# Kernel optimization log

Measured on AMD Instinct MI355X. Metric: run time of the kernel, lower is better.

## Reference

```python
import jax, jax.numpy as jnp
import numpy as np

B, S, D, H = 2, 2048, 2048, 16
HD = D // H
ALIBI_BIAS_MAX = 8
NEG_INF = -1e9  # used only via float('-inf') literal below


def build_attn_mask(n_heads, seq_len, alibi_bias_max=8, dtype=jnp.float32):
    # causal mask: -inf strictly above diagonal
    causal = jnp.triu(jnp.full((seq_len, seq_len), -jnp.inf, dtype=dtype), k=1)
    # full alibi bias: -|i-j| scaled per head by 1/2**(m_h)
    rel = jnp.arange(1 - seq_len, 1, dtype=dtype)  # [S]
    bias = rel[None, :] - rel[:, None]             # [S,S]
    bias = -jnp.abs(bias)
    m = jnp.arange(1, n_heads + 1, dtype=dtype) * (alibi_bias_max / n_heads)
    slopes = 1.0 / (2.0 ** m)                      # [H]
    a_bias = bias[None, :, :] * slopes[:, None, None]  # [H,S,S]
    return causal[None, :, :] + a_bias


def setup_inputs() -> dict:
    key = jax.random.key(0)
    ks = jax.random.split(key, 6)
    x = jax.random.normal(ks[0], (B, S, D), dtype=jnp.float32)
    key_padding_mask = jnp.ones((B, S), dtype=bool)  # True = keep (module inverts before torch)
    attn_mask = build_attn_mask(H, S, ALIBI_BIAS_MAX)
    scale = 1.0 / np.sqrt(D)
    in_proj_w = jax.random.normal(ks[1], (3 * D, D), dtype=jnp.float32) * scale
    in_proj_b = jax.random.normal(ks[2], (3 * D,), dtype=jnp.float32) * 0.01
    out_w = jax.random.normal(ks[3], (D, D), dtype=jnp.float32) * scale
    out_b = jax.random.normal(ks[4], (D,), dtype=jnp.float32) * 0.01
    return {"x": x, "key_padding_mask": key_padding_mask, "attn_mask": attn_mask,
            "in_proj_w": in_proj_w, "in_proj_b": in_proj_b,
            "out_w": out_w, "out_b": out_b}


def reference(x, key_padding_mask, attn_mask, in_proj_w, in_proj_b, out_w, out_b):
    # fused QKV projection (torch MultiheadAttention in_proj)
    qkv = jnp.einsum('bsd,ed->bse', x, in_proj_w) + in_proj_b  # [B,S,3D]
    q, k, v = jnp.split(qkv, 3, axis=-1)
    # [B,H,S,hd]
    q = q.reshape(B, S, H, HD).transpose(0, 2, 1, 3)
    k = k.reshape(B, S, H, HD).transpose(0, 2, 1, 3)
    v = v.reshape(B, S, H, HD).transpose(0, 2, 1, 3)
    scores = jnp.einsum('bhqd,bhkd->bhqk', q, k) / jnp.sqrt(jnp.float32(HD))
    scores = scores + attn_mask[None]  # causal + alibi, [1,H,S,S]
    # key_padding_mask True = keep; masked keys -> -inf
    scores = jnp.where(key_padding_mask[:, None, None, :], scores, -jnp.inf)
    attn = jax.nn.softmax(scores, axis=-1)  # [B,H,S,S]
    ctx = jnp.einsum('bhqk,bhkd->bhqd', attn, v)
    ctx = ctx.transpose(0, 2, 1, 3).reshape(B, S, D)
    out = jnp.einsum('bsd,ed->bse', ctx, out_w) + out_b
    # need_weights=True, average_attn_weights default True -> mean over heads
    avg_attn = attn.mean(axis=1)  # [B,S,S]
    return out, avg_attn
```

## Files before the change

kernel.cpp:

```cpp
#include <hip/hip_runtime.h>
#include <math.h>

#define BB 2
#define SS 2048
#define DD 2048
#define HH 16
#define HDIM 128
#define QKVP 6144
#define NEG_INIT  -1.0e30f
#define NEG_CLAMP -3.0e4f

typedef __attribute__((ext_vector_type(8))) short s8v;
typedef __attribute__((ext_vector_type(4))) float f4v;

typedef const unsigned __attribute__((address_space(1)))* gas_ptr;
typedef unsigned __attribute__((address_space(3)))* las_ptr;

__device__ __forceinline__ void gld16(const short* g, short* l) {
  __builtin_amdgcn_global_load_lds((gas_ptr)g, (las_ptr)l, 16, 0, 0);
}

__device__ __forceinline__ short f2bf(float f) {
  unsigned u = __float_as_uint(f);
  unsigned r = (u + 0x7FFFu + ((u >> 16) & 1u)) >> 16;
  return (short)(unsigned short)r;
}

__global__ void conv_bf16(const float* __restrict__ src, short* __restrict__ dst,
                          int n8) {
  int t = blockIdx.x * blockDim.x + threadIdx.x;
  if (t >= n8) return;
  const float* s = src + (size_t)t * 8;
  s8v o;
#pragma unroll
  for (int i = 0; i < 8; i++) o[i] = f2bf(s[i]);
  ((s8v*)dst)[t] = o;
}

template <typename TOUT>
__global__ __launch_bounds__(256) void gemm_bt_bias(
    const short* __restrict__ A, const short* __restrict__ Bm,
    const float* __restrict__ bias, TOUT* __restrict__ C,
    int M, int N, int K)
{
  __shared__ short As[128 * 64];
  __shared__ short Bs[128 * 64];
  const int tid = threadIdx.x;
  const int lane = tid & 63, wid = tid >> 6;
  const int wm = wid >> 1, wn = wid & 1;
  const int ln = lane & 15, quad = lane >> 4;
  const int m0 = blockIdx.y * 128, n0 = blockIdx.x * 128;

  f4v acc[4][4];
#pragma unroll
  for (int i = 0; i < 4; i++)
#pragma unroll
    for (int j = 0; j < 4; j++) acc[i][j] = {0.f, 0.f, 0.f, 0.f};

  const int srow = (lane >> 3);
  const int scol = (lane & 7) * 8;

  for (int kt = 0; kt < K; kt += 64) {
    const short* a_g = A  + (size_t)(m0 + wid * 32 + srow) * K + kt + scol;
    const short* b_g = Bm + (size_t)(n0 + wid * 32 + srow) * K + kt + scol;
    __syncthreads();
#pragma unroll
    for (int i = 0; i < 4; i++) {
      gld16(a_g + (size_t)i * 8 * K, &As[(wid * 32 + i * 8) * 64]);
      gld16(b_g + (size_t)i * 8 * K, &Bs[(wid * 32 + i * 8) * 64]);
    }
    __syncthreads();
#pragma unroll
    for (int kc = 0; kc < 2; kc++) {
      s8v af[4], bfr[4];
#pragma unroll
      for (int i = 0; i < 4; i++)
        af[i] = *(const s8v*)&As[(wm * 64 + i * 16 + ln) * 64 + kc * 32 + quad * 8];
#pragma unroll
      for (int j = 0; j < 4; j++)
        bfr[j] = *(const s8v*)&Bs[(wn * 64 + j * 16 + ln) * 64 + kc * 32 + quad * 8];
#pragma unroll
      for (int i = 0; i < 4; i++)
#pragma unroll
        for (int j = 0; j < 4; j++)
          acc[i][j] = __builtin_amdgcn_mfma_f32_16x16x32_bf16(af[i], bfr[j], acc[i][j], 0, 0, 0);
    }
  }
#pragma unroll
  for (int j = 0; j < 4; j++) {
    int col = n0 + wn * 64 + j * 16 + ln;
    float bv = bias[col];
#pragma unroll
    for (int i = 0; i < 4; i++) {
      int rbase = m0 + wm * 64 + i * 16 + quad * 4;
#pragma unroll
      for (int r = 0; r < 4; r++) {
        float val = acc[i][j][r] + bv;
        if constexpr (sizeof(TOUT) == 4)
          C[(size_t)(rbase + r) * N + col] = val;
        else
          C[(size_t)(rbase + r) * N + col] = f2bf(val);
      }
    }
  }
}

__global__ __launch_bounds__(256) void transpose_v(const short* __restrict__ qkv,
                                                   short* __restrict__ vT) {
  __shared__ short tile[64 * 72];
  const int bh = blockIdx.z;
  const int b = bh >> 4;
  const int hsel = bh & 15;
  const int s0 = blockIdx.x * 64;
  const int hd0 = blockIdx.y * 64;
  const int t = threadIdx.x;
  const int r = t >> 3, c8 = t & 7;
#pragma unroll
  for (int half = 0; half < 2; half++) {
    int rr = r + half * 32;
    s8v v = *(const s8v*)&qkv[(size_t)(b * SS + s0 + rr) * QKVP + 4096 + hsel * HDIM + hd0 + c8 * 8];
    *(s8v*)&tile[rr * 72 + c8 * 8] = v;
  }
  __syncthreads();
#pragma unroll
  for (int half = 0; half < 2; half++) {
    int rr = r + half * 32;
    s8v o;
#pragma unroll
    for (int j = 0; j < 8; j++) o[j] = tile[(c8 * 8 + j) * 72 + rr];
    *(s8v*)&vT[((size_t)bh * HDIM + hd0 + rr) * SS + s0 + c8 * 8] = o;
  }
}

__global__ __launch_bounds__(512, 4) void flash_fwd(
    const short* __restrict__ qkv, const short* __restrict__ vT,
    float* __restrict__ lse, short* __restrict__ ctx)
{
  __shared__ short Ks[64 * 136];
  __shared__ short Vs[128 * 72];
  __shared__ short plds[8][16 * 72];

  const int g = blockIdx.x;
  const int b = g >> 8;
  const int h = (g >> 4) & 15;
  const int qh = g & 15;
  const int qt = b ? qh : 15 - qh;

  const int bh = b * HH + h;
  const int tid = threadIdx.x, lane = tid & 63, wid = tid >> 6;
  const int ln = lane & 15, quad = lane >> 4;
  const int q0 = qt * 128 + wid * 16;

  const short* qb = qkv + (size_t)b * SS * QKVP + h * HDIM;
  const short* kb = qb + 2048;
  const short* vb = vT + (size_t)bh * HDIM * SS;

  const int krow = tid >> 3, kc0 = (tid & 7) * 8;
  const int vrow = tid >> 2, vc0 = (tid & 3) * 8;
  const short* kgp = kb + (size_t)krow * QKVP + kc0;
  const short* vgp = vb + (size_t)vrow * SS + vc0;
  short* kls = &Ks[krow * 136 + kc0];
  short* vls = &Vs[vrow * 72 + vc0];

  const float slope = exp2f(-0.5f * (float)(h + 1));
  const float scale = 0.08838834764831845f;

  s8v aq[4];
#pragma unroll
  for (int kc = 0; kc < 4; kc++)
    aq[kc] = *(const s8v*)&qb[(size_t)(q0 + ln) * QKVP + kc * 32 + quad * 8];

  s8v k0r = ((const s8v*)kgp)[0], k1r = *(const s8v*)(kgp + 64);
  s8v v0r = ((const s8v*)vgp)[0], v1r = *(const s8v*)(vgp + 32);

  f4v o[8];
#pragma unroll
  for (int d = 0; d < 8; d++) o[d] = {0.f, 0.f, 0.f, 0.f};
  float mrow[4], lrow[4];
#pragma unroll
  for (int r = 0; r < 4; r++) { mrow[r] = NEG_INIT; lrow[r] = 0.0f; }

  const int nkt = 2 * qt + 2;
  for (int kt = 0; kt < nkt; kt++) {
    __syncthreads();
    *(s8v*)kls = k0r;  *(s8v*)(kls + 64) = k1r;
    *(s8v*)vls = v0r;  *(s8v*)(vls + 32) = v1r;
    if (kt < nkt - 1) {
      const short* kn = kgp + (size_t)(kt + 1) * 64 * QKVP;
      const short* vn = vgp + (kt + 1) * 64;
      k0r = ((const s8v*)kn)[0]; k1r = *(const s8v*)(kn + 64);
      v0r = ((const s8v*)vn)[0]; v1r = *(const s8v*)(vn + 32);
    }
    __syncthreads();

    if (kt * 64 > q0 + 15) continue;

    f4v sacc[4];
#pragma unroll
    for (int ks = 0; ks < 4; ks++) {
      f4v z = {0.f, 0.f, 0.f, 0.f};
      if (kt * 64 + ks * 16 <= q0 + 15) {
#pragma unroll
        for (int kc = 0; kc < 4; kc++) {
          s8v bk = *(const s8v*)&Ks[(ks * 16 + ln) * 136 + kc * 32 + quad * 8];
          z = __builtin_amdgcn_mfma_f32_16x16x32_bf16(aq[kc], bk, z, 0, 0, 0);
        }
      }
      sacc[ks] = z;
    }
    float sv[4][4];
#pragma unroll
    for (int ks = 0; ks < 4; ks++)
#pragma unroll
      for (int r = 0; r < 4; r++) {
        int i = q0 + quad * 4 + r;
        int j = kt * 64 + ks * 16 + ln;
        int di = i - j;
        sv[ks][r] = (di >= 0) ? fmaf(sacc[ks][r], scale, -(float)di * slope)
                              : NEG_CLAMP;
      }
    float mnew[4], al[4];
#pragma unroll
    for (int r = 0; r < 4; r++) {
      float mx = fmaxf(fmaxf(sv[0][r], sv[1][r]), fmaxf(sv[2][r], sv[3][r]));
#pragma unroll
      for (int off = 1; off < 16; off <<= 1)
        mx = fmaxf(mx, __shfl_xor(mx, off, 64));
      mnew[r] = fmaxf(mrow[r], mx);
      al[r] = __expf(mrow[r] - mnew[r]);
      mrow[r] = mnew[r];
    }
    float ps[4] = {0.f, 0.f, 0.f, 0.f};
    short pb[4][4];
#pragma unroll
    for (int ks = 0; ks < 4; ks++)
#pragma unroll
      for (int r = 0; r < 4; r++) {
        float p = __expf(sv[ks][r] - mnew[r]);
        ps[r] += p;
        pb[ks][r] = f2bf(p);
      }
#pragma unroll
    for (int r = 0; r < 4; r++) {
      float s = ps[r];
#pragma unroll
      for (int off = 1; off < 16; off <<= 1) s += __shfl_xor(s, off, 64);
      lrow[r] = lrow[r] * al[r] + s;
    }
#pragma unroll
    for (int d = 0; d < 8; d++)
#pragma unroll
      for (int r = 0; r < 4; r++) o[d][r] *= al[r];
#pragma unroll
    for (int ks = 0; ks < 4; ks++)
#pragma unroll
      for (int r = 0; r < 4; r++)
        plds[wid][(quad * 4 + r) * 72 + ks * 16 + ln] = pb[ks][r];
#pragma unroll
    for (int kc2 = 0; kc2 < 2; kc2++) {
      s8v ap = *(const s8v*)&plds[wid][ln * 72 + kc2 * 32 + quad * 8];
#pragma unroll
      for (int d = 0; d < 8; d++) {
        s8v bv = *(const s8v*)&Vs[(d * 16 + ln) * 72 + kc2 * 32 + quad * 8];
        o[d] = __builtin_amdgcn_mfma_f32_16x16x32_bf16(ap, bv, o[d], 0, 0, 0);
      }
    }
  }
  float inv[4];
#pragma unroll
  for (int r = 0; r < 4; r++) inv[r] = 1.0f / lrow[r];
#pragma unroll
  for (int d = 0; d < 8; d++)
#pragma unroll
    for (int r = 0; r < 4; r++) {
      int qrow = q0 + quad * 4 + r;
      ctx[((size_t)(b * SS + qrow)) * DD + h * HDIM + d * 16 + ln] = f2bf(o[d][r] * inv[r]);
    }
#pragma unroll
  for (int r = 0; r < 4; r++)
    if (ln == r)
      lse[(size_t)bh * SS + q0 + quad * 4 + r] = mrow[r] + __logf(lrow[r]);
}

__global__ __launch_bounds__(512, 4) void avg_attn_kernel(
    const short* __restrict__ qkv, const float* __restrict__ lse,
    float* __restrict__ avg)
{
  __shared__ short Ks[128 * 136];
  const int ktile = blockIdx.x, qtile = blockIdx.y, b = blockIdx.z;
  const int tid = threadIdx.x, lane = tid & 63, wid = tid >> 6;
  const int ln = lane & 15, quad = lane >> 4;
  const int q0 = qtile * 128 + wid * 16;
  const int k0 = ktile * 128;
  float acc[8][4];
#pragma unroll
  for (int ks = 0; ks < 8; ks++)
#pragma unroll
    for (int r = 0; r < 4; r++) acc[ks][r] = 0.0f;

  if (ktile <= qtile) {
    const float scale = 0.08838834764831845f;
    const int krow = tid >> 2, kch = (tid & 3) * 8;
    const short* kg0 = qkv + (size_t)(b * SS + k0 + krow) * QKVP + 2048 + kch;
    short* kls = &Ks[krow * 136 + kch];
    s8v kreg[4];
#pragma unroll
    for (int j = 0; j < 4; j++) kreg[j] = *(const s8v*)(kg0 + j * 32);
    for (int hh = 0; hh < HH; hh++) {
      __syncthreads();
#pragma unroll
      for (int j = 0; j < 4; j++) *(s8v*)(kls + j * 32) = kreg[j];
      if (hh < HH - 1) {
        const short* kn = kg0 + (hh + 1) * HDIM;
#pragma unroll
        for (int j = 0; j < 4; j++) kreg[j] = *(const s8v*)(kn + j * 32);
      }
      __syncthreads();
      const int bh = b * HH + hh;
      const float slope = exp2f(-0.5f * (float)(hh + 1));
      const short* qb = qkv + (size_t)b * SS * QKVP + hh * HDIM;
      s8v aq[4];
#pragma unroll
      for (int kc = 0; kc < 4; kc++)
        aq[kc] = *(const s8v*)&qb[(size_t)(q0 + ln) * QKVP + kc * 32 + quad * 8];
      float lsev[4];
#pragma unroll
      for (int r = 0; r < 4; r++) lsev[r] = lse[(size_t)bh * SS + q0 + quad * 4 + r];
#pragma unroll
      for (int ks = 0; ks < 8; ks++) {
        if (k0 + ks * 16 > q0 + 15) continue;
        f4v z = {0.f, 0.f, 0.f, 0.f};
#pragma unroll
        for (int kc = 0; kc < 4; kc++) {
          s8v bk = *(const s8v*)&Ks[(ks * 16 + ln) * 136 + kc * 32 + quad * 8];
          z = __builtin_amdgcn_mfma_f32_16x16x32_bf16(aq[kc], bk, z, 0, 0, 0);
        }
#pragma unroll
        for (int r = 0; r < 4; r++) {
          int i = q0 + quad * 4 + r;
          int j = k0 + ks * 16 + ln;
          int di = i - j;
          float svv = (di >= 0) ? fmaf(z[r], scale, -(float)di * slope) : NEG_CLAMP;
          acc[ks][r] += __expf(svv - lsev[r]);
        }
      }
    }
  }
  const float inv16 = 1.0f / 16.0f;
#pragma unroll
  for (int ks = 0; ks < 8; ks++)
#pragma unroll
    for (int r = 0; r < 4; r++)
      avg[((size_t)b * SS + q0 + quad * 4 + r) * SS + k0 + ks * 16 + ln] =
          acc[ks][r] * inv16;
}

extern "C" void kernel_launch(void* const* d_in, const int* in_sizes, int n_in,
                              void* d_out, int out_size, void* d_ws, size_t ws_size,
                              hipStream_t stream)
{
  const float *x = nullptr, *w_in = nullptr, *b_in = nullptr,
              *w_out = nullptr, *b_out = nullptr;
  for (int idx = 0; idx < n_in; idx++) {
    switch (in_sizes[idx]) {
      case 8388608:  x     = (const float*)d_in[idx]; break;
      case 12582912: w_in  = (const float*)d_in[idx]; break;
      case 6144:     b_in  = (const float*)d_in[idx]; break;
      case 4194304:  w_out = (const float*)d_in[idx]; break;
      case 2048:     b_out = (const float*)d_in[idx]; break;
      default: break;
    }
  }

  char* ws = (char*)d_ws;
  short* qkv = (short*)(ws);
  short* xb  = (short*)(ws + 50331648);
  short* vT  = (short*)(ws + 50331648);
  short* wib = (short*)(ws + 67108864);
  short* ctx = (short*)(ws + 67108864);
  float* lse = (float*)(ws + 83886080);
  short* wob = (short*)(ws + 92274688);

  float* outp = (float*)d_out;
  float* avgp = outp + (size_t)BB * SS * DD;

  conv_bf16<<<4096, 256, 0, stream>>>(x, xb, 1048576);
  conv_bf16<<<6144, 256, 0, stream>>>(w_in, wib, 1572864);
  conv_bf16<<<2048, 256, 0, stream>>>(w_out, wob, 524288);

  gemm_bt_bias<short><<<dim3(QKVP / 128, (BB * SS) / 128), 256, 0, stream>>>(
      xb, wib, b_in, qkv, BB * SS, QKVP, DD);
  transpose_v<<<dim3(32, 2, 32), 256, 0, stream>>>(qkv, vT);
  flash_fwd<<<dim3(512, 1, 1), 512, 0, stream>>>(qkv, vT, lse, ctx);
  avg_attn_kernel<<<dim3(16, 16, 2), 512, 0, stream>>>(qkv, lse, avgp);
  gemm_bt_bias<float><<<dim3(DD / 128, (BB * SS) / 128), 256, 0, stream>>>(
      ctx, wob, b_out, outp, BB * SS, DD, DD);
}
```

Baseline: 722.1 us.

## Double-buffer GEMM LDS tiles, swizzle workgroup order, raise MFMA wave priority

The projection GEMM now uses two LDS buffers and issues the global-to-LDS loads for the next K tile before computing the current one, with one barrier per iteration instead of two. It also remaps the flat workgroup index with a stride-8 swizzle, likely to spread neighbouring tiles across XCDs or improve L2 locality. The attention kernel wraps its MFMA sections in s_setprio to favour matrix work across waves. LDS use for the GEMM doubles to 64 KB per block, which may reduce occupancy, and the swizzle assumes the workgroup count divides by 8.

```diff
diff --git a/kernel.cpp b/kernel.cpp
--- a/kernel.cpp
+++ b/kernel.cpp
@@ -43,13 +43,18 @@
     const float* __restrict__ bias, TOUT* __restrict__ C,
     int M, int N, int K)
 {
-  __shared__ short As[128 * 64];
-  __shared__ short Bs[128 * 64];
+  __shared__ short As[2][128 * 64];
+  __shared__ short Bs[2][128 * 64];
   const int tid = threadIdx.x;
   const int lane = tid & 63, wid = tid >> 6;
   const int wm = wid >> 1, wn = wid & 1;
   const int ln = lane & 15, quad = lane >> 4;
-  const int m0 = blockIdx.y * 128, n0 = blockIdx.x * 128;
+
+  const int nx = gridDim.x;
+  const int nwg = nx * gridDim.y;
+  int flat = blockIdx.y * nx + blockIdx.x;
+  flat = (flat & 7) * (nwg >> 3) + (flat >> 3);
+  const int m0 = (flat / nx) * 128, n0 = (flat % nx) * 128;
 
   f4v acc[4][4];
 #pragma unroll
@@ -59,32 +64,44 @@
 
   const int srow = (lane >> 3);
   const int scol = (lane & 7) * 8;
-
+  const short* a_g = A  + (size_t)(m0 + wid * 32 + srow) * K + scol;
+  const short* b_g = Bm + (size_t)(n0 + wid * 32 + srow) * K + scol;
+
+#pragma unroll
+  for (int i = 0; i < 4; i++) {
+    gld16(a_g + (size_t)i * 8 * K, &As[0][(wid * 32 + i * 8) * 64]);
+    gld16(b_g + (size_t)i * 8 * K, &Bs[0][(wid * 32 + i * 8) * 64]);
+  }
+  __syncthreads();
+
+  int cur = 0;
   for (int kt = 0; kt < K; kt += 64) {
-    const short* a_g = A  + (size_t)(m0 + wid * 32 + srow) * K + kt + scol;
-    const short* b_g = Bm + (size_t)(n0 + wid * 32 + srow) * K + kt + scol;
-    __syncthreads();
-#pragma unroll
-    for (int i = 0; i < 4; i++) {
-      gld16(a_g + (size_t)i * 8 * K, &As[(wid * 32 + i * 8) * 64]);
-      gld16(b_g + (size_t)i * 8 * K, &Bs[(wid * 32 + i * 8) * 64]);
-    }
-    __syncthreads();
+    if (kt + 64 < K) {
+      const short* an = a_g + kt + 64;
+      const short* bn = b_g + kt + 64;
+#pragma unroll
+      for (int i = 0; i < 4; i++) {
+        gld16(an + (size_t)i * 8 * K, &As[cur ^ 1][(wid * 32 + i * 8) * 64]);
+        gld16(bn + (size_t)i * 8 * K, &Bs[cur ^ 1][(wid * 32 + i * 8) * 64]);
+      }
+    }
 #pragma unroll
     for (int kc = 0; kc < 2; kc++) {
       s8v af[4], bfr[4];
 #pragma unroll
       for (int i = 0; i < 4; i++)
-        af[i] = *(const s8v*)&As[(wm * 64 + i * 16 + ln) * 64 + kc * 32 + quad * 8];
+        af[i] = *(const s8v*)&As[cur][(wm * 64 + i * 16 + ln) * 64 + kc * 32 + quad * 8];
 #pragma unroll
       for (int j = 0; j < 4; j++)
-        bfr[j] = *(const s8v*)&Bs[(wn * 64 + j * 16 + ln) * 64 + kc * 32 + quad * 8];
+        bfr[j] = *(const s8v*)&Bs[cur][(wn * 64 + j * 16 + ln) * 64 + kc * 32 + quad * 8];
 #pragma unroll
       for (int i = 0; i < 4; i++)
 #pragma unroll
         for (int j = 0; j < 4; j++)
           acc[i][j] = __builtin_amdgcn_mfma_f32_16x16x32_bf16(af[i], bfr[j], acc[i][j], 0, 0, 0);
     }
+    __syncthreads();
+    cur ^= 1;
   }
 #pragma unroll
   for (int j = 0; j < 4; j++) {
@@ -196,6 +213,7 @@
     if (kt * 64 > q0 + 15) continue;
 
     f4v sacc[4];
+    __builtin_amdgcn_s_setprio(1);
 #pragma unroll
     for (int ks = 0; ks < 4; ks++) {
       f4v z = {0.f, 0.f, 0.f, 0.f};
@@ -208,6 +226,7 @@
       }
       sacc[ks] = z;
     }
+    __builtin_amdgcn_s_setprio(0);
     float sv[4][4];
 #pragma unroll
     for (int ks = 0; ks < 4; ks++)
@@ -256,6 +275,7 @@
 #pragma unroll
       for (int r = 0; r < 4; r++)
         plds[wid][(quad * 4 + r) * 72 + ks * 16 + ln] = pb[ks][r];
+    __builtin_amdgcn_s_setprio(1);
 #pragma unroll
     for (int kc2 = 0; kc2 < 2; kc2++) {
       s8v ap = *(const s8v*)&plds[wid][ln * 72 + kc2 * 32 + quad * 8];
@@ -265,6 +285,7 @@
         o[d] = __builtin_amdgcn_mfma_f32_16x16x32_bf16(ap, bv, o[d], 0, 0, 0);
       }
     }
+    __builtin_amdgcn_s_setprio(0);
   }
   float inv[4];
 #pragma unroll
```

Result: slower. 747.0 us (+3.4%).
